# Performance work log

Measured on AMD Instinct MI355X. Metric: run time of the kernel, lower is better.

The kernel has to match this reference:

```python
import jax, jax.numpy as jnp
import numpy as np

B = 64          # batch
N = 256         # input_dim (number of MPS sites / pixels)
BOND = 128      # bond dimension
DF = 2          # feature dimension per pixel
OUT = 10        # output classes
EPS = 1e-12


def _xavier_uniform(key, shape, fan_in, fan_out, gain):
    bound = gain * np.sqrt(6.0 / (fan_in + fan_out))
    return jax.random.uniform(key, shape, jnp.float32, -bound, bound)


def setup_inputs() -> dict:
    key = jax.random.key(0)
    k_x, k_c0, k_cr, k_cl = jax.random.split(key, 4)
    gain = float(np.sqrt(2.0 / (1.0 + 0.01 ** 2)))  # leaky_relu gain
    x = jax.random.uniform(k_x, (B, N), dtype=jnp.float32)  # pixels in [0,1]
    # core 0: (1, DF, BOND); torch fan_in = DF*BOND, fan_out = 1*BOND
    core0 = _xavier_uniform(k_c0, (1, DF, BOND), DF * BOND, BOND, gain)
    # remaining N-1 cores: (BOND, DF, BOND); fan_in = DF*BOND, fan_out = BOND*BOND... torch: fan_in = shape[1]*shape[2] = DF*BOND, fan_out = shape[0]*shape[2] = BOND*BOND? No: fan_out = shape[0]*prod(shape[2:]) = BOND*BOND
    cores = _xavier_uniform(k_cr, (N - 1, BOND, DF, BOND), DF * BOND, BOND * BOND, gain)
    classifier = _xavier_uniform(k_cl, (OUT, BOND), BOND, OUT, gain)
    return {"x": x, "core0": core0, "cores": cores, "classifier": classifier}


def _mps_forward(x, core0, cores, classifier):
    b = x.shape[0]
    H = core0.shape[-1]
    # feature map: pixel v -> (1-v, v)
    feats = jnp.stack([1.0 - x, x], axis=-1)                  # (B, N, DF)
    # contract each core with its pixel feature
    special = jnp.einsum('ldh,bd->blh', core0, feats[:, 0])   # (B, 1, H)
    others = jnp.einsum('nldh,bnd->bnlh', cores, feats[:, 1:])  # (B, N-1, H, H)
    log_norm = jnp.zeros((b,), dtype=x.dtype)

    # log-depth tree contraction; loop bound is static (trace-time)
    while 1 + others.shape[1] > 1:
        # pad the special (1,H) leftmost tensor up to (H,H) with zero rows
        padded = jnp.pad(special, ((0, 0), (0, H - special.shape[1]), (0, 0)))
        full = jnp.concatenate([padded[:, None], others], axis=1)  # (B, K, H, H)
        K = full.shape[1]
        odd = (K % 2 != 0)
        if odd:
            last = full[:, -1]
            full = full[:, :-1]
        s1 = full[:, 0::2]                                    # (B, P, H, H)
        s2 = full[:, 1::2]
        cp = jnp.matmul(s1, s2)                               # (B, P, H, H)
        norms = jnp.maximum(
            jnp.sqrt(jnp.sum(cp * cp, axis=(-2, -1))), EPS)   # (B, P)
        log_norm = log_norm + jnp.sum(jnp.log(norms), axis=1)
        cp = cp / norms[:, :, None, None]
        special = cp[:, 0, 0:1, :]                            # keep only row 0
        others = cp[:, 1:]
        if odd:
            others = jnp.concatenate([others, last[:, None]], axis=1)

    mps_out = special[:, 0, :]                                # (B, H)
    logits = mps_out @ classifier.T + log_norm[:, None]      # (B, OUT)
    return logits


def reference(x, core0, cores, classifier):
    return _mps_forward(x, core0, cores, classifier)
```

## Files before the change

### kernel.cpp

```cpp
#include <hip/hip_runtime.h>
#include <stdint.h>


typedef unsigned short u16;
typedef __attribute__((ext_vector_type(8))) short short8;
typedef __attribute__((ext_vector_type(4))) float f32x4;

#define HP 136

__device__ __forceinline__ u16 f2b(float f) {
  uint32_t u = __builtin_bit_cast(uint32_t, f);
  u += 0x7FFFu + ((u >> 16) & 1u);
  return (u16)(u >> 16);
}
__device__ __forceinline__ float b2f(u16 b) {
  uint32_t u = ((uint32_t)b) << 16;
  return __builtin_bit_cast(float, u);
}

struct AccW { f32x4 t[2][2]; };

__device__ __forceinline__ void mfma_w16(const u16* Alds, const u16* Blds,
                                         AccW& acc) {
  const int tid = threadIdx.x;
  const int wid = tid >> 6, lane = tid & 63;
  const int wm = (wid >> 2) * 32, wn = (wid & 3) * 32;
  const int l16 = lane & 15, quad = lane >> 4;
#pragma unroll
  for (int tm = 0; tm < 2; tm++)
#pragma unroll
    for (int tn = 0; tn < 2; tn++)
      acc.t[tm][tn] = (f32x4){0.f, 0.f, 0.f, 0.f};
#pragma unroll
  for (int kk = 0; kk < 128; kk += 32) {
    short8 af[2], bf[2];
#pragma unroll
    for (int t = 0; t < 2; t++) {
      af[t] = *(const short8*)(Alds + (wm + t * 16 + l16) * HP + kk + quad * 8);
      bf[t] = *(const short8*)(Blds + (wn + t * 16 + l16) * HP + kk + quad * 8);
    }
#pragma unroll
    for (int tm = 0; tm < 2; tm++)
#pragma unroll
      for (int tn = 0; tn < 2; tn++)
        acc.t[tm][tn] = __builtin_amdgcn_mfma_f32_16x16x32_bf16(
            af[tm], bf[tn], acc.t[tm][tn], 0, 0, 0);
  }
}

__device__ __forceinline__ float acc_sumsq(const AccW& acc) {
  float ss = 0.f;
#pragma unroll
  for (int tm = 0; tm < 2; tm++)
#pragma unroll
    for (int tn = 0; tn < 2; tn++)
#pragma unroll
      for (int i = 0; i < 4; i++) {
        float v = acc.t[tm][tn][i];
        ss += v * v;
      }
  return ss;
}

__device__ __forceinline__ void bounce_store(u16* Lb, const AccW& acc, float scale,
                                             bool transposed) {
  const int tid = threadIdx.x;
  const int wid = tid >> 6, lane = tid & 63;
  const int wm = (wid >> 2) * 32, wn = (wid & 3) * 32;
  const int l16 = lane & 15, quad = lane >> 4;
#pragma unroll
  for (int tm = 0; tm < 2; tm++)
#pragma unroll
    for (int tn = 0; tn < 2; tn++)
#pragma unroll
      for (int i = 0; i < 4; i++) {
        int r = wm + tm * 16 + quad * 4 + i;
        int c = wn + tn * 16 + l16;
        int key = transposed ? c : r, sec = transposed ? r : c;
        Lb[key * HP + sec] = f2b(acc.t[tm][tn][i] * scale);
      }
}

__device__ __forceinline__ void copy_out(const u16* Lb, u16* out) {
  const int tid = threadIdx.x;
#pragma unroll
  for (int i = 0; i < 2; i++) {
    int g8 = tid + i * 1024;
    int row = g8 >> 4, c8 = g8 & 15;
    *(uint4*)(out + g8 * 8) = *(const uint4*)(Lb + row * HP + c8 * 8);
  }
}

__device__ __forceinline__ void loadM(u16* Lb, const u16* __restrict__ src) {
  const int tid = threadIdx.x;
#pragma unroll
  for (int i = 0; i < 2; i++) {
    int g8 = tid + i * 1024;
    int r = g8 >> 4, c8 = g8 & 15;
    *(uint4*)(Lb + r * HP + c8 * 8) = *(const uint4*)(src + g8 * 8);
  }
}

__device__ __forceinline__ float block_sum(float v, float* red, int nw) {
#pragma unroll
  for (int off = 32; off > 0; off >>= 1) v += __shfl_down(v, off);
  int wid = threadIdx.x >> 6;
  if ((threadIdx.x & 63) == 0) red[wid] = v;
  __syncthreads();
  if (threadIdx.x == 0) {
    float s = 0.f;
    for (int w = 0; w < nw; w++) s += red[w];
    red[0] = s;
  }
  __syncthreads();
  float s = red[0];
  __syncthreads();
  return s;
}

__device__ __forceinline__ float bsum16(float v, float* red) {
#pragma unroll
  for (int off = 32; off > 0; off >>= 1) v += __shfl_down(v, off);
  if ((threadIdx.x & 63) == 0) red[threadIdx.x >> 6] = v;
  __syncthreads();
  float s = 0.f;
#pragma unroll
  for (int w = 0; w < 16; w++) s += red[w];
  return s;
}

__global__ __launch_bounds__(1024) void k1(const float* __restrict__ cores,
                                           u16* __restrict__ T) {
  __shared__ u16 Ald[128 * HP], B0[128 * HP], B1[128 * HP];
  const int j = blockIdx.x;
  const int p = blockIdx.y;
  const float* c1 = cores + (size_t)(2 * j + 1) * 32768;
  const float* c2 = cores + (size_t)(2 * j + 2) * 32768;
  const int tid = threadIdx.x;
#pragma unroll 4
  for (int i = 0; i < 16; i++) {
    int lh = tid + i * 1024;
    int l = lh >> 7, h = lh & 127;
    float a0 = c1[(l * 2 + 0) * 128 + h];
    float av = p ? (c1[(l * 2 + 1) * 128 + h] - a0) : a0;
    Ald[l * HP + h] = f2b(av);
    float b0 = c2[(l * 2 + 0) * 128 + h];
    float b1 = c2[(l * 2 + 1) * 128 + h];
    B0[h * HP + l] = f2b(b0);
    B1[h * HP + l] = f2b(b1 - b0);
  }
  __syncthreads();
  const bool tr = (j % 2) == 0;
  u16* Tj = T + ((size_t)j * 4 + p * 2) * 16384;
  AccW q0, q1;
  mfma_w16(Ald, B0, q0);
  mfma_w16(Ald, B1, q1);
  __syncthreads();
  bounce_store(Ald, q0, 1.f, tr); __syncthreads();
  copy_out(Ald, Tj + 0 * 16384);  __syncthreads();
  bounce_store(Ald, q1, 1.f, tr); __syncthreads();
  copy_out(Ald, Tj + 1 * 16384);
}

__global__ __launch_bounds__(1024, 8) void k1b(const u16* __restrict__ T,
                                               u16* __restrict__ TT) {
  __shared__ u16 Ald[128 * HP], Bld[128 * HP];
  const int t = blockIdx.x;
  const int j2 = blockIdx.y;
  const int m1 = 2 * j2 + 1, m2 = 2 * j2 + 2;
  const u16* TA = T + ((size_t)m1 * 4 + (t >> 2)) * 16384;
  const u16* TB = T + ((size_t)m2 * 4 + (t & 3)) * 16384;
  loadM(Ald, TA);
  loadM(Bld, TB);
  __syncthreads();
  AccW acc;
  mfma_w16(Ald, Bld, acc);
  __syncthreads();
  bounce_store(Ald, acc, 1.f, (j2 % 2) == 0);
  __syncthreads();
  copy_out(Ald, TT + ((size_t)j2 * 16 + t) * 16384);
}

__global__ __launch_bounds__(256) void k1c(const u16* __restrict__ TT,
                                           float* __restrict__ Gpart) {
  __shared__ float Gp[1024];
  const int j2 = blockIdx.x, kc = blockIdx.y;
  const int tid = threadIdx.x;
  const int w = tid >> 6, lane = tid & 63;
  const int l16 = lane & 15, quad = lane >> 4;
  const u16* V = TT + (size_t)j2 * 16 * 16384 + (size_t)l16 * 16384;
  const int k0 = kc * 4096 + w * 1024;
  f32x4 acc = (f32x4){0.f, 0.f, 0.f, 0.f};
  for (int kk = k0; kk < k0 + 1024; kk += 32) {
    short8 av = *(const short8*)(V + kk + quad * 8);
    acc = __builtin_amdgcn_mfma_f32_16x16x32_bf16(av, av, acc, 0, 0, 0);
  }
#pragma unroll
  for (int i = 0; i < 4; i++)
    Gp[w * 256 + (quad * 4 + i) * 16 + l16] = acc[i];
  __syncthreads();
  Gpart[((size_t)j2 * 4 + kc) * 256 + tid] =
      Gp[tid] + Gp[256 + tid] + Gp[512 + tid] + Gp[768 + tid];
}

__global__ __launch_bounds__(128) void k2ns(const float* __restrict__ x,
                                            const float* __restrict__ Gpart,
                                            const float* __restrict__ core0,
                                            const float* __restrict__ cores,
                                            const u16* __restrict__ T,
                                            float* __restrict__ cbuf,
                                            float* __restrict__ sA,
                                            float* __restrict__ logs) {
  __shared__ float Gs[256];
  __shared__ float svec[128];
  __shared__ float red[8];
  const int bx = blockIdx.x, tid = threadIdx.x;
  if (bx < 63) {
    const int j2 = bx;
#pragma unroll
    for (int i = 0; i < 2; i++) {
      int t2 = tid + i * 128;
      float s = 0.f;
#pragma unroll
      for (int kc = 0; kc < 4; kc++)
        s += Gpart[((size_t)j2 * 4 + kc) * 256 + t2];
      Gs[t2] = s;
    }
    __syncthreads();
    if (tid < 64) {
      const int b = tid;
      const float* xb = x + b * 256;
      const int m1 = 2 * j2 + 1, m2 = 2 * j2 + 2;
      float a1 = xb[2 * m1 + 2], b1 = xb[2 * m1 + 3];
      float a2 = xb[2 * m2 + 2], b2 = xb[2 * m2 + 3];
      float c1[4] = {1.f, b1, a1, a1 * b1};
      float c2[4] = {1.f, b2, a2, a2 * b2};
      float c[16];
#pragma unroll
      for (int p = 0; p < 4; p++)
#pragma unroll
        for (int q = 0; q < 4; q++) c[p * 4 + q] = c1[p] * c2[q];
      float n2 = 0.f;
#pragma unroll
      for (int t = 0; t < 16; t++) {
        float s = 0.f;
#pragma unroll
        for (int u = 0; u < 16; u++) s += Gs[t * 16 + u] * c[u];
        n2 += c[t] * s;
      }
      float n = fmaxf(sqrtf(n2), 1e-12f);
      logs[b * 127 + 1 + j2] = logf(n);
      float inv = 1.f / n;
#pragma unroll
      for (int t = 0; t < 16; t++)
        cbuf[((size_t)j2 * 64 + b) * 16 + t] = c[t] * inv;
    }
  } else {
    const int b = bx - 63;
    const float* xb = x + b * 256;
    float x0 = xb[0], x1 = xb[1];
    svec[tid] = core0[tid] * (1.f - x0) + core0[128 + tid] * x0;
    __syncthreads();
    float acc1 = 0.f;
    for (int k = 0; k < 128; k++) {
      float m0 = cores[(k * 2 + 0) * 128 + tid];
      float m1 = cores[(k * 2 + 1) * 128 + tid];
      acc1 += svec[k] * (m0 + x1 * (m1 - m0));
    }
    float tot = block_sum(acc1 * acc1, red, 2);
    float n1 = fmaxf(sqrtf(tot), 1e-12f);
    float ln = logf(n1);
    svec[tid] = acc1 / n1;
    __syncthreads();
    float a = xb[2], bb = xb[3], ab = a * bb;
    float acc2 = 0.f;
    for (int k8 = 0; k8 < 16; k8++) {
      union { uint4 v; u16 s[8]; } q00, q01, q10, q11;
      q00.v = *(const uint4*)(T + tid * 128 + k8 * 8);
      q01.v = *(const uint4*)(T + 16384 + tid * 128 + k8 * 8);
      q10.v = *(const uint4*)(T + 32768 + tid * 128 + k8 * 8);
      q11.v = *(const uint4*)(T + 49152 + tid * 128 + k8 * 8);
#pragma unroll
      for (int e = 0; e < 8; e++) {
        float pk = b2f(q00.s[e]) + a * b2f(q10.s[e]) + bb * b2f(q01.s[e]) +
                   ab * b2f(q11.s[e]);
        acc2 += svec[k8 * 8 + e] * pk;
      }
    }
    float tot2 = block_sum(acc2 * acc2, red, 2);
    float n2 = fmaxf(sqrtf(tot2), 1e-12f);
    sA[b * 128 + tid] = acc2 / n2;
    if (tid == 0) logs[b * 127 + 0] = ln + logf(n2);
  }
}

__global__ __launch_bounds__(256, 4) void k2c(const u16* __restrict__ TT,
                                              const float* __restrict__ cbuf,
                                              u16* __restrict__ M0) {
  const int slice = blockIdx.x;
  const int j2 = blockIdx.y;
  const int tid = threadIdx.x;
  const int e0 = slice * 512 + tid * 2;
  float v[16][2];
#pragma unroll
  for (int t = 0; t < 16; t++) {
    union { uint32_t u; u16 s[2]; } q;
    q.u = *(const uint32_t*)(TT + ((size_t)j2 * 16 + t) * 16384 + e0);
    v[t][0] = b2f(q.s[0]);
    v[t][1] = b2f(q.s[1]);
  }
  const float4* cb4 = (const float4*)(cbuf + (size_t)j2 * 1024);
  u16* out = M0 + (size_t)j2 * 16384 + e0;
#pragma unroll 4
  for (int b = 0; b < 64; b++) {
    float4 c0 = cb4[b * 4 + 0];
    float4 c1 = cb4[b * 4 + 1];
    float4 c2 = cb4[b * 4 + 2];
    float4 c3 = cb4[b * 4 + 3];
    float cc[16] = {c0.x, c0.y, c0.z, c0.w, c1.x, c1.y, c1.z, c1.w,
                    c2.x, c2.y, c2.z, c2.w, c3.x, c3.y, c3.z, c3.w};
    float o0 = 0.f, o1 = 0.f;
#pragma unroll
    for (int t = 0; t < 16; t++) {
      o0 += cc[t] * v[t][0];
      o1 += cc[t] * v[t][1];
    }
    union { uint32_t u; u16 s[2]; } r;
    r.s[0] = f2b(o0);
    r.s[1] = f2b(o1);
    *(uint32_t*)(out + (size_t)b * 63 * 16384) = r.u;
  }
}

__device__ __forceinline__ AccW subtree3n(const u16* __restrict__ base, int midx,
                                          u16* L0, u16* L1, float* red,
                                          float* logs, int b, float& nOut) {
  loadM(L0, base + (size_t)(4 * midx + 3) * 16384);
  loadM(L1, base + (size_t)(4 * midx + 4) * 16384);
  __syncthreads();
  AccW a1;
  mfma_w16(L0, L1, a1);
  __syncthreads();
  loadM(L0, base + (size_t)(4 * midx + 5) * 16384);
  loadM(L1, base + (size_t)(4 * midx + 6) * 16384);
  __syncthreads();
  AccW a2;
  mfma_w16(L0, L1, a2);
  __syncthreads();
  bounce_store(L0, a1, 1.f, false);
  bounce_store(L1, a2, 1.f, true);
  if (threadIdx.x == 0) {
    logs[b * 127 + 66 + 2 * midx] = 0.f;
    logs[b * 127 + 67 + 2 * midx] = 0.f;
  }
  __syncthreads();
  AccW a3;
  mfma_w16(L0, L1, a3);
  float t = bsum16(acc_sumsq(a3), red);
  float n = fmaxf(sqrtf(t), 1e-12f);
  if (threadIdx.x == 0) logs[b * 127 + 97 + midx] = logf(n);
  nOut = n;
  return a3;
}

__global__ __launch_bounds__(1024, 4) void tree(const u16* __restrict__ In,
                                                u16* __restrict__ Out,
                                                const float* __restrict__ sIn,
                                                float* __restrict__ sOut,
                                                float* __restrict__ logs) {
  __shared__ u16 L0[128 * HP], L1[128 * HP], L2[128 * HP], L3[128 * HP];
  __shared__ float svf[256];
  __shared__ float red[16];
  const int b = blockIdx.y, p = blockIdx.x, tid = threadIdx.x;
  const u16* base = In + (size_t)b * 63 * 16384;
  if (p < 3) {
    const int m = p;
    float n1, n2, n3, n4;
    AccW t1 = subtree3n(base, 4 * m + 3, L0, L1, red, logs, b, n1);
    bounce_store(L2, t1, 1.f / n1, false);
    AccW t2 = subtree3n(base, 4 * m + 4, L0, L1, red, logs, b, n2);
    bounce_store(L3, t2, 1.f / n2, true);
    __syncthreads();
    AccW pa;
    mfma_w16(L2, L3, pa);
    __syncthreads();
    bounce_store(L2, pa, 1.f, false);
    AccW t3 = subtree3n(base, 4 * m + 5, L0, L1, red, logs, b, n3);
    bounce_store(L3, t3, 1.f / n3, false);
    AccW t4 = subtree3n(base, 4 * m + 6, L0, L1, red, logs, b, n4);
    bounce_store(L0, t4, 1.f / n4, true);
    if (tid == 0) {
      logs[b * 127 + 114 + 2 * m] = 0.f;
      logs[b * 127 + 115 + 2 * m] = 0.f;
    }
    __syncthreads();
    AccW pb;
    mfma_w16(L3, L0, pb);
    __syncthreads();
    bounce_store(L1, pb, 1.f, true);
    __syncthreads();
    AccW f;
    mfma_w16(L2, L1, f);
    float tF = bsum16(acc_sumsq(f), red);
    float nF = fmaxf(sqrtf(tF), 1e-12f);
    if (tid == 0) logs[b * 127 + 121 + m] = logf(nF);
    bounce_store(L3, f, 1.f / nF, (m % 2) == 0);
    __syncthreads();
    copy_out(L3, Out + ((size_t)b * 3 + m) * 16384);
  } else {
    if (tid < 128) svf[tid] = sIn[b * 128 + tid];
    loadM(L0, base + 1 * 16384);
    loadM(L1, base + 2 * 16384);
    __syncthreads();
    float acc0 = 0.f;
    if (tid < 128) {
      for (int k8 = 0; k8 < 16; k8++) {
        union { uint4 v; u16 s[8]; } q;
        q.v = *(const uint4*)(base + tid * 128 + k8 * 8);
#pragma unroll
        for (int e = 0; e < 8; e++) acc0 += svf[k8 * 8 + e] * b2f(q.s[e]);
      }
    }
    AccW q1;
    mfma_w16(L0, L1, q1);
    __syncthreads();
    bounce_store(L0, q1, 1.f, true);
    if (tid < 128) svf[128 + tid] = acc0;
    if (tid == 0) {
      logs[b * 127 + 64] = 0.f;
      logs[b * 127 + 65] = 0.f;
    }
    __syncthreads();
    float acc2 = 0.f;
    if (tid < 128) {
      for (int l = 0; l < 128; l++) acc2 += svf[128 + l] * b2f(L0[tid * HP + l]);
    }
    float t2s = bsum16((tid < 128) ? acc2 * acc2 : 0.f, red);
    float nv2 = fmaxf(sqrtf(t2s), 1e-12f);
    if (tid == 0) logs[b * 127 + 96] = logf(nv2);
    if (tid < 128) svf[tid] = acc2 / nv2;
    __syncthreads();
    float n0s, n1s, n2s;
    AccW s0 = subtree3n(base, 0, L0, L1, red, logs, b, n0s);
    bounce_store(L2, s0, 1.f / n0s, true);
    __syncthreads();
    float acc3 = 0.f;
    if (tid < 128) {
      for (int l = 0; l < 128; l++) acc3 += svf[l] * b2f(L2[tid * HP + l]);
    }
    if (tid < 128) svf[128 + tid] = acc3;
    __syncthreads();
    AccW s1 = subtree3n(base, 1, L0, L1, red, logs, b, n1s);
    bounce_store(L2, s1, 1.f / n1s, false);
    AccW s2 = subtree3n(base, 2, L0, L1, red, logs, b, n2s);
    bounce_store(L3, s2, 1.f / n2s, true);
    if (tid == 0) {
      logs[b * 127 + 112] = 0.f;
      logs[b * 127 + 113] = 0.f;
    }
    __syncthreads();
    AccW q2;
    mfma_w16(L2, L3, q2);
    __syncthreads();
    bounce_store(L2, q2, 1.f, true);
    __syncthreads();
    float acc4 = 0.f;
    if (tid < 128) {
      for (int l = 0; l < 128; l++) acc4 += svf[128 + l] * b2f(L2[tid * HP + l]);
    }
    float t4s = bsum16((tid < 128) ? acc4 * acc4 : 0.f, red);
    float nv4 = fmaxf(sqrtf(t4s), 1e-12f);
    if (tid == 0) logs[b * 127 + 120] = logf(nv4);
    if (tid < 128) sOut[b * 128 + tid] = acc4 / nv4;
  }
}

__global__ __launch_bounds__(1024, 8) void r7f(const u16* __restrict__ In,
                                               const float* __restrict__ sIn,
                                               const float* __restrict__ logs,
                                               const float* __restrict__ cls,
                                               float* __restrict__ out) {
  __shared__ u16 Ald[128 * HP], Bld[128 * HP];
  __shared__ float svec[128], ovec[128], red[16];
  const int b = blockIdx.x, tid = threadIdx.x;
  if (tid < 128) svec[tid] = sIn[b * 128 + tid];
  loadM(Ald, In + ((size_t)b * 3 + 1) * 16384);
  loadM(Bld, In + ((size_t)b * 3 + 2) * 16384);
  __syncthreads();
  AccW acc;
  mfma_w16(Ald, Bld, acc);
  const u16* M0p = In + (size_t)b * 3 * 16384;
  float acc0 = 0.f;
  if (tid < 128) {
    for (int k8 = 0; k8 < 16; k8++) {
      union { uint4 v; u16 s[8]; } q;
      q.v = *(const uint4*)(M0p + tid * 128 + k8 * 8);
#pragma unroll
      for (int e = 0; e < 8; e++) acc0 += svec[k8 * 8 + e] * b2f(q.s[e]);
    }
  }
  __syncthreads();
  bounce_store(Ald, acc, 1.f, true);
  if (tid < 128) ovec[tid] = acc0;
  __syncthreads();
  float acc2 = 0.f;
  if (tid < 128) {
    for (int r = 0; r < 128; r++) acc2 += ovec[r] * b2f(Ald[tid * HP + r]);
  }
  float tot = bsum16((tid < 128) ? acc2 * acc2 : 0.f, red);
  float n = fmaxf(sqrtf(tot), 1e-12f);
  float lg = logf(n);
  if (tid < 128) svec[tid] = acc2 / n;
  __syncthreads();
  if (tid < 10) {
    float a = 0.f;
    for (int h = 0; h < 128; h++) a += svec[h] * cls[tid * 128 + h];
    float L = lg;
    for (int i = 0; i < 124; i++) L += logs[b * 127 + i];
    out[b * 10 + tid] = a + L;
  }
}

extern "C" void kernel_launch(void* const* d_in, const int* in_sizes, int n_in,
                              void* d_out, int out_size, void* d_ws, size_t ws_size,
                              hipStream_t stream) {
  (void)in_sizes; (void)n_in; (void)out_size; (void)ws_size;
  const float* x     = (const float*)d_in[0];
  const float* core0 = (const float*)d_in[1];
  const float* cores = (const float*)d_in[2];
  const float* cls   = (const float*)d_in[3];
  float* out = (float*)d_out;
  char* ws = (char*)d_ws;

  constexpr size_t SZ_T  = (size_t)127 * 4 * 16384 * 2;
  constexpr size_t SZ_A  = (size_t)64 * 31 * 16384 * 2;
  constexpr size_t SZ_M0 = (size_t)64 * 63 * 16384 * 2;

  u16*   T    = (u16*)(ws);
  u16*   TT   = (u16*)(ws + SZ_T);
  u16*   M4   = (u16*)(ws);
  u16*   M0   = (u16*)(ws + SZ_A);
  char*  tail0 = ws + SZ_A + SZ_M0;
  float* Gpart = (float*)(tail0);
  float* cbuf = (float*)(tail0 + 262144);
  float* sA   = (float*)(tail0 + 262144 + 262144);
  float* sB   = (float*)(tail0 + 262144 + 262144 + 32768);
  float* logs = (float*)(tail0 + 262144 + 262144 + 65536);

  k1  <<<dim3(127, 2), 1024, 0, stream>>>(cores, T);
  k1b <<<dim3(16, 63), 1024, 0, stream>>>(T, TT);
  k1c <<<dim3(63, 4), 256, 0, stream>>>(TT, Gpart);
  k2ns<<<dim3(127), 128, 0, stream>>>(x, Gpart, core0, cores, T, cbuf, sA, logs);
  k2c <<<dim3(32, 63), 256, 0, stream>>>(TT, cbuf, M0);
  tree<<<dim3(4, 64), 1024, 0, stream>>>(M0, M4, sA, sB, logs);
  r7f <<<dim3(64), 1024, 0, stream>>>(M4, sB, logs, cls, out);
}
```

Baseline: 227.6 us.

## Load four leaf matrices at once in subtrees and use non-transposed vector-matrix reads

The subtree helper now loads all four leaf matrices into four LDS buffers up front and runs both leaf products back-to-back. This removes a barrier and a serialized global-load round between them. The callers are reordered so intermediate results stay in registers across subtree calls and are written back afterward. The vector-matrix loops now store matrices untransposed and read them column-wise, so adjacent threads hit adjacent LDS addresses. The cost is more LDS in use at once and longer live ranges for the accumulators, which adds register pressure.

Measured after the change: 231.2 us. About the same (+1.6%).

```diff
diff --git a/kernel.cpp b/kernel.cpp
--- a/kernel.cpp
+++ b/kernel.cpp
@@ -332,20 +332,19 @@
   }
 }
 
-__device__ __forceinline__ AccW subtree3n(const u16* __restrict__ base, int midx,
-                                          u16* L0, u16* L1, float* red,
-                                          float* logs, int b, float& nOut) {
+__device__ __forceinline__ AccW subtree4n(const u16* __restrict__ base, int midx,
+                                          u16* L0, u16* L1, u16* L2, u16* L3,
+                                          float* red, float* logs, int b,
+                                          float& nOut) {
   loadM(L0, base + (size_t)(4 * midx + 3) * 16384);
   loadM(L1, base + (size_t)(4 * midx + 4) * 16384);
+  loadM(L2, base + (size_t)(4 * midx + 5) * 16384);
+  loadM(L3, base + (size_t)(4 * midx + 6) * 16384);
   __syncthreads();
   AccW a1;
   mfma_w16(L0, L1, a1);
-  __syncthreads();
-  loadM(L0, base + (size_t)(4 * midx + 5) * 16384);
-  loadM(L1, base + (size_t)(4 * midx + 6) * 16384);
-  __syncthreads();
   AccW a2;
-  mfma_w16(L0, L1, a2);
+  mfma_w16(L2, L3, a2);
   __syncthreads();
   bounce_store(L0, a1, 1.f, false);
   bounce_store(L1, a2, 1.f, true);
@@ -376,37 +375,36 @@
   if (p < 3) {
     const int m = p;
     float n1, n2, n3, n4;
-    AccW t1 = subtree3n(base, 4 * m + 3, L0, L1, red, logs, b, n1);
-    bounce_store(L2, t1, 1.f / n1, false);
-    AccW t2 = subtree3n(base, 4 * m + 4, L0, L1, red, logs, b, n2);
-    bounce_store(L3, t2, 1.f / n2, true);
+    AccW r1 = subtree4n(base, 4 * m + 3, L0, L1, L2, L3, red, logs, b, n1);
+    AccW r2 = subtree4n(base, 4 * m + 4, L0, L1, L2, L3, red, logs, b, n2);
+    bounce_store(L2, r1, 1.f / n1, false);
+    bounce_store(L3, r2, 1.f / n2, true);
     __syncthreads();
     AccW pa;
     mfma_w16(L2, L3, pa);
     __syncthreads();
-    bounce_store(L2, pa, 1.f, false);
-    AccW t3 = subtree3n(base, 4 * m + 5, L0, L1, red, logs, b, n3);
-    bounce_store(L3, t3, 1.f / n3, false);
-    AccW t4 = subtree3n(base, 4 * m + 6, L0, L1, red, logs, b, n4);
-    bounce_store(L0, t4, 1.f / n4, true);
+    AccW r3 = subtree4n(base, 4 * m + 5, L0, L1, L2, L3, red, logs, b, n3);
+    AccW r4 = subtree4n(base, 4 * m + 6, L0, L1, L2, L3, red, logs, b, n4);
+    bounce_store(L2, r3, 1.f / n3, false);
+    bounce_store(L3, r4, 1.f / n4, true);
     if (tid == 0) {
       logs[b * 127 + 114 + 2 * m] = 0.f;
       logs[b * 127 + 115 + 2 * m] = 0.f;
     }
     __syncthreads();
     AccW pb;
-    mfma_w16(L3, L0, pb);
-    __syncthreads();
+    mfma_w16(L2, L3, pb);
+    bounce_store(L0, pa, 1.f, false);
     bounce_store(L1, pb, 1.f, true);
     __syncthreads();
     AccW f;
-    mfma_w16(L2, L1, f);
+    mfma_w16(L0, L1, f);
     float tF = bsum16(acc_sumsq(f), red);
     float nF = fmaxf(sqrtf(tF), 1e-12f);
     if (tid == 0) logs[b * 127 + 121 + m] = logf(nF);
-    bounce_store(L3, f, 1.f / nF, (m % 2) == 0);
-    __syncthreads();
-    copy_out(L3, Out + ((size_t)b * 3 + m) * 16384);
+    bounce_store(L2, f, 1.f / nF, (m % 2) == 0);
+    __syncthreads();
+    copy_out(L2, Out + ((size_t)b * 3 + m) * 16384);
   } else {
     if (tid < 128) svf[tid] = sIn[b * 128 + tid];
     loadM(L0, base + 1 * 16384);
@@ -424,7 +422,7 @@
     AccW q1;
     mfma_w16(L0, L1, q1);
     __syncthreads();
-    bounce_store(L0, q1, 1.f, true);
+    bounce_store(L0, q1, 1.f, false);
     if (tid < 128) svf[128 + tid] = acc0;
     if (tid == 0) {
       logs[b * 127 + 64] = 0.f;
@@ -433,7 +431,7 @@
     __syncthreads();
     float acc2 = 0.f;
     if (tid < 128) {
-      for (int l = 0; l < 128; l++) acc2 += svf[128 + l] * b2f(L0[tid * HP + l]);
+      for (int l = 0; l < 128; l++) acc2 += svf[128 + l] * b2f(L0[l * HP + tid]);
     }
     float t2s = bsum16((tid < 128) ? acc2 * acc2 : 0.f, red);
     float nv2 = fmaxf(sqrtf(t2s), 1e-12f);
@@ -441,18 +439,18 @@
     if (tid < 128) svf[tid] = acc2 / nv2;
     __syncthreads();
     float n0s, n1s, n2s;
-    AccW s0 = subtree3n(base, 0, L0, L1, red, logs, b, n0s);
-    bounce_store(L2, s0, 1.f / n0s, true);
+    AccW s0 = subtree4n(base, 0, L0, L1, L2, L3, red, logs, b, n0s);
+    bounce_store(L2, s0, 1.f / n0s, false);
     __syncthreads();
     float acc3 = 0.f;
     if (tid < 128) {
-      for (int l = 0; l < 128; l++) acc3 += svf[l] * b2f(L2[tid * HP + l]);
+      for (int l = 0; l < 128; l++) acc3 += svf[l] * b2f(L2[l * HP + tid]);
     }
     if (tid < 128) svf[128 + tid] = acc3;
     __syncthreads();
-    AccW s1 = subtree3n(base, 1, L0, L1, red, logs, b, n1s);
+    AccW s1 = subtree4n(base, 1, L0, L1, L2, L3, red, logs, b, n1s);
+    AccW s2 = subtree4n(base, 2, L0, L1, L2, L3, red, logs, b, n2s);
     bounce_store(L2, s1, 1.f / n1s, false);
-    AccW s2 = subtree3n(base, 2, L0, L1, red, logs, b, n2s);
     bounce_store(L3, s2, 1.f / n2s, true);
     if (tid == 0) {
       logs[b * 127 + 112] = 0.f;
@@ -462,11 +460,11 @@
     AccW q2;
     mfma_w16(L2, L3, q2);
     __syncthreads();
-    bounce_store(L2, q2, 1.f, true);
+    bounce_store(L2, q2, 1.f, false);
     __syncthreads();
     float acc4 = 0.f;
     if (tid < 128) {
-      for (int l = 0; l < 128; l++) acc4 += svf[128 + l] * b2f(L2[tid * HP + l]);
+      for (int l = 0; l < 128; l++) acc4 += svf[128 + l] * b2f(L2[l * HP + tid]);
     }
     float t4s = bsum16((tid < 128) ? acc4 * acc4 : 0.f, red);
     float nv4 = fmaxf(sqrtf(t4s), 1e-12f);
@@ -500,12 +498,12 @@
     }
   }
   __syncthreads();
-  bounce_store(Ald, acc, 1.f, true);
+  bounce_store(Ald, acc, 1.f, false);
   if (tid < 128) ovec[tid] = acc0;
   __syncthreads();
   float acc2 = 0.f;
   if (tid < 128) {
-    for (int r = 0; r < 128; r++) acc2 += ovec[r] * b2f(Ald[tid * HP + r]);
+    for (int r = 0; r < 128; r++) acc2 += ovec[r] * b2f(Ald[r * HP + tid]);
   }
   float tot = bsum16((tid < 128) ? acc2 * acc2 : 0.f, red);
   float n = fmaxf(sqrtf(tot), 1e-12f);
```
